# Optimization experiments

Hardware: AMD Instinct MI355X
Metric: run time of the kernel (lower is better)

Reference implementation:

```python
import jax, jax.numpy as jnp
import numpy as np

S, B, NS, NC = 128, 64, 128, 8
D, Z, H, HI, NF = 32, 64, 128, 128, 2
N = NS * B
LOG2PI = float(np.log(2.0 * np.pi))
_m_in = np.arange(1, Z + 1)
_m_hid = (np.arange(HI) % (Z - 1)) + 1
MASK1 = jnp.asarray((_m_hid[None, :] >= _m_in[:, None]).astype(np.float32))  # [Z,HI]
MASK2 = jnp.asarray((_m_in[None, :] > _m_hid[:, None]).astype(np.float32))   # [HI,Z]


def setup_inputs() -> dict:
    key = jax.random.key(0)
    ks = jax.random.split(key, 16)
    r = lambda i, shape: jax.random.normal(ks[i], shape, jnp.float32) * 0.1
    return dict(
        input=jax.random.normal(ks[0], (S, B, D), jnp.float32),
        eps=jax.random.normal(ks[1], (S, N, Z), jnp.float32),
        u=jax.random.uniform(ks[2], (S, 3, NC, NS, B), dtype=jnp.float32),
        Wxh=r(3, (D, H)), Wzh=r(4, (Z, H)), bh=jnp.zeros(H, jnp.float32),
        Wg=r(5, (H, Z)), bg=jnp.zeros(Z, jnp.float32),
        Wp=r(6, (H, Z)), bp=jnp.zeros(Z, jnp.float32),
        Wz=r(7, (Z, Z)), bz=jnp.zeros(Z, jnp.float32),
        Wsc=r(8, (Z, Z)), bsc=jnp.zeros(Z, jnp.float32),
        iaf_W1=r(9, (NF, Z, HI)), iaf_b1=jnp.zeros((NF, HI), jnp.float32),
        iaf_Wm=r(10, (NF, HI, Z)), iaf_bm=jnp.zeros((NF, Z), jnp.float32),
        iaf_Ws=r(11, (NF, HI, Z)), iaf_bs=jnp.zeros((NF, Z), jnp.float32),
        We1=r(12, (Z, H)), be1=jnp.zeros(H, jnp.float32),
        We2=r(13, (H, 4 * NC)), be2=jnp.zeros(4 * NC, jnp.float32),
    )


def _forward(input, eps, u, Wxh, Wzh, bh, Wg, bg, Wp, bp, Wz, bz, Wsc, bsc,
             iaf_W1, iaf_b1, iaf_Wm, iaf_bm, iaf_Ws, iaf_bs, We1, be1, We2, be2):
    def step(z_prev, inp):
        x, eps_t, u_t = inp                        # x:[B,D] eps_t:[N,Z] u_t:[3,NC,NS,B]
        xr = jnp.tile(x, (NS, 1))                  # == input[i].repeat(n_samples, 1) -> [N,D]
        # GatedTransition
        h = jax.nn.relu(xr @ Wxh + z_prev @ Wzh + bh)
        gate = jax.nn.sigmoid(h @ Wg + bg)
        prop = h @ Wp + bp
        loc = (1.0 - gate) * (z_prev @ Wz + bz) + gate * prop
        scale = jax.nn.softplus(jax.nn.relu(prop) @ Wsc + bsc) + 1e-3
        # base rsample + log_prob of base sample (eps form)
        z = loc + scale * eps_t
        base_lp = jnp.sum(-0.5 * eps_t * eps_t - jnp.log(scale) - 0.5 * LOG2PI, axis=-1)
        # IAF stack: y = sigma*x + (1-sigma)*mu, cached log_prob = base_lp - sum log sigma
        logdet = jnp.zeros((N,), z.dtype)
        for f in range(NF):
            hh = jax.nn.relu(z @ (iaf_W1[f] * MASK1) + iaf_b1[f])
            mu = hh @ (iaf_Wm[f] * MASK2) + iaf_bm[f]
            sg = jax.nn.sigmoid(hh @ (iaf_Ws[f] * MASK2) + iaf_bs[f] + 1.0)
            z = sg * z + (1.0 - sg) * mu
            logdet = logdet + jnp.sum(jnp.log(sg), axis=-1)
        z_lp = (base_lp - logdet).reshape(NS, B)
        # Emitter -> [N, 4*NC]; .t().view(4,NC,NS,B).split([3,1])
        e = jax.nn.relu(z @ We1 + be1) @ We2 + be2
        et = e.T.reshape(4, NC, NS, B)
        logits, frac = et[:3], jax.nn.sigmoid(et[3:4])
        samp = (u_t < jax.nn.sigmoid(logits)).astype(jnp.float32)  # Bernoulli sample
        x_lp = samp * jax.nn.log_sigmoid(logits) + (1.0 - samp) * jax.nn.log_sigmoid(-logits)
        return z, (samp, frac, x_lp, z_lp)

    z0 = jnp.zeros((N, Z), input.dtype)
    _, (samples, fractions, x_logprobs, z_logprobs) = jax.lax.scan(step, z0, (input, eps, u))
    return samples, fractions, x_logprobs, z_logprobs


def reference(input, eps, u, Wxh, Wzh, bh, Wg, bg, Wp, bp, Wz, bz, Wsc, bsc,
              iaf_W1, iaf_b1, iaf_Wm, iaf_bm, iaf_Ws, iaf_bs, We1, be1, We2, be2):
    return _forward(input, eps, u, Wxh, Wzh, bh, Wg, bg, Wp, bp, Wz, bz, Wsc, bsc,
                    iaf_W1, iaf_b1, iaf_Wm, iaf_bm, iaf_Ws, iaf_bs, We1, be1, We2, be2)
```

## Files before the change

kernel.cpp:

```cpp
#include <hip/hip_runtime.h>


typedef _Float16 f16x8 __attribute__((ext_vector_type(8)));
typedef _Float16 f16x4 __attribute__((ext_vector_type(4)));
typedef float    f32x4 __attribute__((ext_vector_type(4)));
typedef unsigned short u16;

#define MFMA16(a,b,c) __builtin_amdgcn_mfma_f32_16x16x32_f16((a),(b),(c),0,0,0)

namespace {
constexpr int S = 128;
constexpr long FRAC_OFF = 25165824L;
constexpr long XLP_OFF  = 33554432L;
constexpr long ZLP_OFF  = 58720256L;
constexpr float HLOG2PI = 0.91893853320467274f;
constexpr float INVLO   = 1.0f / 2048.0f;

constexpr int C1HI = 0,      C1LO = 12288;
constexpr int GPHI = 24576,  GPLO = 40960;
constexpr int WZHI = 57344,  WZLO = 61440;
constexpr int SCHI = 65536,  SCLO = 69632;
constexpr int W1B  = 73728;
constexpr int MSB  = 106496;
constexpr int E1HI = 172032, E1LO = 180224;
constexpr int E2HI = 188416, E2LO = 192512;
constexpr int XHI  = 196608, XLO  = 458752;
}

__device__ __forceinline__ float sigm(float x)      { return 1.0f / (1.0f + __expf(-x)); }
__device__ __forceinline__ float softplusf_(float x){ return fmaxf(x, 0.f) + __logf(1.f + __expf(-fabsf(x))); }
__device__ __forceinline__ float logsigm(float x)   { return fminf(x, 0.f) - __logf(1.f + __expf(-fabsf(x))); }

__device__ __forceinline__ void split2(float v, _Float16& hi, _Float16& lo) {
    hi = (_Float16)v;
    lo = (_Float16)((v - (float)hi) * 2048.0f);
}

__device__ __forceinline__ f16x8 rdA(const u16* t, int row, int k, int strideEls, int swm) {
    int byte = ((row * strideEls + k) * 2) ^ ((row & swm) << 4);
    return *(const f16x8*)((const char*)t + byte);
}
__device__ __forceinline__ f16x8 ldB(const u16* wa, int base, int col, int K, int koff) {
    return *(const f16x8*)(wa + base + col * K + koff);
}
__device__ __forceinline__ f16x8 ldLo(const u16* lds, int el, int col) {
    int byte = (el * 2) ^ ((col & 7) << 4);
    return *(const f16x8*)((const char*)lds + byte);
}

template<int NKS, int STRIDE, int SWM>
__device__ __forceinline__ void mmDual(const u16* Th, const u16* Tl, int lnc, int kf,
                                       const f16x8 (&wh)[NKS], const f16x8 (&wl)[NKS],
                                       float bias, f32x4& H0, f32x4& L0, f32x4& H1, f32x4& L1)
{
    H0 = (f32x4){bias, bias, bias, bias}; H1 = H0;
    L0 = (f32x4){0.f, 0.f, 0.f, 0.f};     L1 = L0;
#pragma unroll
    for (int ks = 0; ks < NKS; ++ks) {
        int k = ks * 32 + kf;
        f16x8 a0h = rdA(Th, lnc,      k, STRIDE, SWM);
        f16x8 a0l = rdA(Tl, lnc,      k, STRIDE, SWM);
        f16x8 a1h = rdA(Th, 16 + lnc, k, STRIDE, SWM);
        f16x8 a1l = rdA(Tl, 16 + lnc, k, STRIDE, SWM);
        H0 = MFMA16(a0h, wh[ks], H0); L0 = MFMA16(a0h, wl[ks], L0); L0 = MFMA16(a0l, wh[ks], L0);
        H1 = MFMA16(a1h, wh[ks], H1); L1 = MFMA16(a1h, wl[ks], L1); L1 = MFMA16(a1l, wh[ks], L1);
    }
}

template<bool RELU>
__device__ __forceinline__ void stAct(f32x4 H, f32x4 L, int rt, int lng, int col,
                                      u16* th, u16* tl, int strideEls, int swm)
{
#pragma unroll
    for (int q = 0; q < 4; ++q) {
        int row = rt * 16 + lng * 4 + q;
        float v = H[q] + L[q] * INVLO;
        if (RELU) v = fmaxf(v, 0.f);
        _Float16 hi, lo; split2(v, hi, lo);
        int byte = ((row * strideEls + col) * 2) ^ ((row & swm) << 4);
        *(_Float16*)((char*)th + byte) = hi;
        *(_Float16*)((char*)tl + byte) = lo;
    }
}
__device__ __forceinline__ void stScr(f32x4 H, f32x4 L, int rt, int lng, int col,
                                      float* s, int strideEls)
{
#pragma unroll
    for (int q = 0; q < 4; ++q) {
        int row = rt * 16 + lng * 4 + q;
        int byte = ((row * strideEls + col) * 4) ^ ((row & 7) << 4);
        *(float*)((char*)s + byte) = H[q] + L[q] * INVLO;
    }
}
__device__ __forceinline__ f32x4 rdS4(const float* s, int strideEls, int row, int c) {
    int byte = ((row * strideEls + c) * 4) ^ ((row & 7) << 4);
    return *(const f32x4*)((const char*)s + byte);
}
__device__ __forceinline__ float rdS1(const float* s, int strideEls, int row, int c) {
    int byte = ((row * strideEls + c) * 4) ^ ((row & 7) << 4);
    return *(const float*)((const char*)s + byte);
}
__device__ __forceinline__ void wrS4(float* s, int strideEls, int row, int c, f32x4 v) {
    int byte = ((row * strideEls + c) * 4) ^ ((row & 7) << 4);
    *(f32x4*)((char*)s + byte) = v;
}
__device__ __forceinline__ void wrF16x4(u16* t, int strideEls, int row, int c, f16x4 v) {
    int byte = ((row * strideEls + c) * 2) ^ ((row & 7) << 4);
    *(f16x4*)((char*)t + byte) = v;
}
__device__ __forceinline__ f16x4 rdF16x4(const u16* t, int strideEls, int row, int c) {
    int byte = ((row * strideEls + c) * 2) ^ ((row & 7) << 4);
    return *(const f16x4*)((const char*)t + byte);
}

__global__ void prep_kernel(const float* __restrict__ input,
                            const float* __restrict__ Wxh, const float* __restrict__ Wzh,
                            const float* __restrict__ Wg,  const float* __restrict__ Wp,
                            const float* __restrict__ Wz,  const float* __restrict__ Wsc,
                            const float* __restrict__ W1,  const float* __restrict__ Wm,
                            const float* __restrict__ Ws_, const float* __restrict__ We1,
                            const float* __restrict__ We2, u16* __restrict__ wa)
{
    int idx = blockIdx.x * 256 + threadIdx.x;
    if (idx < 98304) {
        int hio = 0, loo = 0; float v = 0.f;
        int i = idx;
        if (i < 12288) {
            int col = i / 96, k = i % 96;
            v = (k < 32) ? Wxh[k * 128 + col] : Wzh[(k - 32) * 128 + col];
            hio = C1HI + i; loo = C1LO + i;
        } else if (i < 28672) { int j = i - 12288;
            int col = j >> 7, k = j & 127;
            v = (col < 64) ? Wg[k * 64 + col] : Wp[k * 64 + col - 64];
            hio = GPHI + j; loo = GPLO + j;
        } else if (i < 32768) { int j = i - 28672;
            int col = j >> 6, k = j & 63; v = Wz[k * 64 + col];
            hio = WZHI + j; loo = WZLO + j;
        } else if (i < 36864) { int j = i - 32768;
            int col = j >> 6, k = j & 63; v = Wsc[k * 64 + col];
            hio = SCHI + j; loo = SCLO + j;
        } else if (i < 53248) { int j = i - 36864;
            int f = j >> 13, jj = j & 8191;
            int col = jj >> 6, k = jj & 63;
            v = W1[(f * 64 + k) * 128 + col] * (((col % 63) >= k) ? 1.f : 0.f);
            hio = W1B + f * 16384 + jj; loo = hio + 8192;
        } else if (i < 86016) { int j = i - 53248;
            int f = j >> 14, jj = j & 16383;
            int col = jj >> 7, k = jj & 127;
            if (col < 64) v = Wm[(f * 128 + k) * 64 + col] * (((k % 63) < col) ? 1.f : 0.f);
            else { int c = col - 64;
                   v = Ws_[(f * 128 + k) * 64 + c]         * (((k % 63) < c)   ? 1.f : 0.f); }
            hio = MSB + f * 32768 + jj; loo = hio + 16384;
        } else if (i < 94208) { int j = i - 86016;
            int col = j >> 6, k = j & 63; v = We1[k * 128 + col];
            hio = E1HI + j; loo = E1LO + j;
        } else { int j = i - 94208;
            int col = j >> 7, k = j & 127; v = We2[k * 32 + col];
            hio = E2HI + j; loo = E2LO + j;
        }
        _Float16 hi, lo; split2(v, hi, lo);
        wa[hio] = __builtin_bit_cast(u16, hi);
        wa[loo] = __builtin_bit_cast(u16, lo);
    } else {
        int j = idx - 98304;
        if (j < 262144) {
            float v = input[j];
            _Float16 hi, lo; split2(v, hi, lo);
            wa[XHI + j] = __builtin_bit_cast(u16, hi);
            wa[XLO + j] = __builtin_bit_cast(u16, lo);
        }
    }
}

__global__ __launch_bounds__(512, 2)
void ssm_mfma_kernel(const float* __restrict__ eps, const float* __restrict__ u,
                     const float* __restrict__ bh,  const float* __restrict__ bg,
                     const float* __restrict__ bp,  const float* __restrict__ bz,
                     const float* __restrict__ bsc, const float* __restrict__ b1,
                     const float* __restrict__ bm,  const float* __restrict__ bs,
                     const float* __restrict__ be1, const float* __restrict__ be2,
                     const u16* __restrict__ wa, float* __restrict__ out)
{
    __shared__ u16 tXh[32 * 32],  tXl[32 * 32];
    __shared__ u16 tZh[32 * 64],  tZl[32 * 64];
    __shared__ u16 tHh[32 * 128], tHl[32 * 128];
    __shared__ u16 tPh[32 * 64],  tPl[32 * 64];
    __shared__ float scrB[32 * 128];
    __shared__ float scrZ[32 * 64];
    __shared__ float lpS[32][16];
    __shared__ u16 loMS[32768];
    __shared__ u16 loGP[16384];

    const int tid = threadIdx.x;
    const int ln  = tid & 63, w = tid >> 6;
    const int lnc = ln & 15, lng = ln >> 4;
    const int r0  = blockIdx.x * 32, b0 = r0 & 63;
    const int kf  = lng * 8;
    const int col0  = w * 16 + lnc;
    const int colz  = (w & 3) * 16 + lnc;
    const int colE2 = (w & 1) * 16 + lnc;
    const int khE2  = w >> 1;
    const int crow  = tid >> 4, ccol4 = (tid & 15) * 4;
    const int erow  = tid & 31, c0 = (tid >> 5) * 2;

    for (int i8 = tid; i8 < 4096; i8 += 512) {
        int el = i8 * 8;
        int f = el >> 14, rem = el & 16383, col = rem >> 7;
        f16x8 v = *(const f16x8*)(wa + MSB + f * 32768 + 16384 + rem);
        int byte = (el * 2) ^ ((col & 7) << 4);
        *(f16x8*)((char*)loMS + byte) = v;
    }
    for (int i8 = tid; i8 < 2048; i8 += 512) {
        int el = i8 * 8;
        int col = el >> 7;
        f16x8 v = *(const f16x8*)(wa + GPLO + el);
        int byte = (el * 2) ^ ((col & 7) << 4);
        *(f16x8*)((char*)loGP + byte) = v;
    }

    f16x8 wC1h[3], wC1l[3], wGPh[4], wZSh[2], wZSl[2];
    f16x8 wW1h[2][2], wW1l[2][2], wMSh[2][4];
    f16x8 wE1h[2], wE1l[2], wE2h[1], wE2l[1];
#pragma unroll
    for (int ks = 0; ks < 3; ++ks) {
        wC1h[ks] = ldB(wa, C1HI, col0, 96, ks * 32 + kf);
        wC1l[ks] = ldB(wa, C1LO, col0, 96, ks * 32 + kf);
    }
#pragma unroll
    for (int ks = 0; ks < 4; ++ks) {
        wGPh[ks] = ldB(wa, GPHI, col0, 128, ks * 32 + kf);
    }
    if (w < 4) {
#pragma unroll
        for (int ks = 0; ks < 2; ++ks) {
            wZSh[ks] = ldB(wa, WZHI, colz, 64, ks * 32 + kf);
            wZSl[ks] = ldB(wa, WZLO, colz, 64, ks * 32 + kf);
        }
    } else {
#pragma unroll
        for (int ks = 0; ks < 2; ++ks) {
            wZSh[ks] = ldB(wa, SCHI, colz, 64, ks * 32 + kf);
            wZSl[ks] = ldB(wa, SCLO, colz, 64, ks * 32 + kf);
        }
    }
#pragma unroll
    for (int f = 0; f < 2; ++f) {
#pragma unroll
        for (int ks = 0; ks < 2; ++ks) {
            wW1h[f][ks] = ldB(wa, W1B + f * 16384,        col0, 64, ks * 32 + kf);
            wW1l[f][ks] = ldB(wa, W1B + f * 16384 + 8192, col0, 64, ks * 32 + kf);
        }
#pragma unroll
        for (int ks = 0; ks < 4; ++ks) {
            wMSh[f][ks] = ldB(wa, MSB + f * 32768, col0, 128, ks * 32 + kf);
        }
    }
#pragma unroll
    for (int ks = 0; ks < 2; ++ks) {
        wE1h[ks] = ldB(wa, E1HI, col0, 64, ks * 32 + kf);
        wE1l[ks] = ldB(wa, E1LO, col0, 64, ks * 32 + kf);
    }
    wE2h[0] = ldB(wa, E2HI, colE2, 128, khE2 * 32 + kf);
    wE2l[0] = ldB(wa, E2LO, colE2, 128, khE2 * 32 + kf);

    const float bhv  = bh[col0];
    const float bGPv = (col0 < 64) ? bg[col0] : bp[col0 - 64];
    const float bzsv = (w < 4) ? bz[colz] : bsc[colz];
    float bW1v[2], bMSv[2];
#pragma unroll
    for (int f = 0; f < 2; ++f) {
        bW1v[f] = b1[f * 128 + col0];
        bMSv[f] = (col0 < 64) ? bm[f * 64 + col0] : bs[f * 64 + col0 - 64];
    }
    const float bE1v = be1[col0];
    const float bE2v = (khE2 == 0) ? be2[colE2] : 0.f;

    for (int i = tid; i < 32 * 64; i += 512) { tZh[i] = 0; tZl[i] = 0; }
    {
        int rr = tid >> 4, d2 = (tid & 15) * 2;
        int ge = (b0 + rr) * 32 + d2;
        unsigned xh = *(const unsigned*)(wa + XHI + ge);
        unsigned xl = *(const unsigned*)(wa + XLO + ge);
        int byte = (rr * 64 + d2 * 2) ^ ((rr & 3) << 4);
        *(unsigned*)((char*)tXh + byte) = xh;
        *(unsigned*)((char*)tXl + byte) = xl;
    }
    __syncthreads();

    for (int t = 0; t < S; ++t) {
        f32x4 epsv;

        {
            f32x4 H0 = {bhv, bhv, bhv, bhv}, H1 = H0;
            f32x4 L0 = {0.f, 0.f, 0.f, 0.f}, L1 = L0;
            {
                f16x8 a0h = rdA(tXh, lnc, kf, 32, 3),      a0l = rdA(tXl, lnc, kf, 32, 3);
                f16x8 a1h = rdA(tXh, 16 + lnc, kf, 32, 3), a1l = rdA(tXl, 16 + lnc, kf, 32, 3);
                H0 = MFMA16(a0h, wC1h[0], H0); L0 = MFMA16(a0h, wC1l[0], L0); L0 = MFMA16(a0l, wC1h[0], L0);
                H1 = MFMA16(a1h, wC1h[0], H1); L1 = MFMA16(a1h, wC1l[0], L1); L1 = MFMA16(a1l, wC1h[0], L1);
            }
#pragma unroll
            for (int ks = 1; ks < 3; ++ks) {
                int k = (ks - 1) * 32 + kf;
                f16x8 a0h = rdA(tZh, lnc, k, 64, 7),      a0l = rdA(tZl, lnc, k, 64, 7);
                f16x8 a1h = rdA(tZh, 16 + lnc, k, 64, 7), a1l = rdA(tZl, 16 + lnc, k, 64, 7);
                H0 = MFMA16(a0h, wC1h[ks], H0); L0 = MFMA16(a0h, wC1l[ks], L0); L0 = MFMA16(a0l, wC1h[ks], L0);
                H1 = MFMA16(a1h, wC1h[ks], H1); L1 = MFMA16(a1h, wC1l[ks], L1); L1 = MFMA16(a1l, wC1h[ks], L1);
            }
            stAct<true>(H0, L0, 0, lng, col0, tHh, tHl, 128, 7);
            stAct<true>(H1, L1, 1, lng, col0, tHh, tHl, 128, 7);
        }
        if (w < 4) {
            f32x4 H0, L0, H1, L1;
            mmDual<2, 64, 7>(tZh, tZl, lnc, kf, wZSh, wZSl, bzsv, H0, L0, H1, L1);
            stScr(H0, L0, 0, lng, colz, scrZ, 64);
            stScr(H1, L1, 1, lng, colz, scrZ, 64);
        }
        __syncthreads();

        {
            f32x4 H0 = {bGPv, bGPv, bGPv, bGPv}, H1 = H0;
            f32x4 L0 = {0.f, 0.f, 0.f, 0.f}, L1 = L0;
#pragma unroll
            for (int ks = 0; ks < 4; ++ks) {
                int k = ks * 32 + kf;
                f16x8 a0h = rdA(tHh, lnc, k, 128, 7),      a0l = rdA(tHl, lnc, k, 128, 7);
                f16x8 a1h = rdA(tHh, 16 + lnc, k, 128, 7), a1l = rdA(tHl, 16 + lnc, k, 128, 7);
                f16x8 bhf = wGPh[ks];
                f16x8 blf = ldLo(loGP, col0 * 128 + k, col0);
                H0 = MFMA16(a0h, bhf, H0); L0 = MFMA16(a0h, blf, L0); L0 = MFMA16(a0l, bhf, L0);
                H1 = MFMA16(a1h, bhf, H1); L1 = MFMA16(a1h, blf, L1); L1 = MFMA16(a1l, bhf, L1);
            }
            stScr(H0, L0, 0, lng, col0, scrB, 128);
            stScr(H1, L1, 1, lng, col0, scrB, 128);
        }
        __syncthreads();

        {
            epsv = *(const f32x4*)(eps + ((size_t)t * 8192 + r0 + crow) * 64 + ccol4);
            f32x4 gp4 = rdS4(scrB, 128, crow, ccol4);
            f32x4 pr4 = rdS4(scrB, 128, crow, 64 + ccol4);
            f32x4 zw4 = rdS4(scrZ, 64, crow, ccol4);
            f32x4 loc4; f16x4 ph4, pl4;
#pragma unroll
            for (int i = 0; i < 4; ++i) {
                float g = sigm(gp4[i]);
                loc4[i] = (1.f - g) * zw4[i] + g * pr4[i];
                float rp = fmaxf(pr4[i], 0.f);
                _Float16 hi, lo; split2(rp, hi, lo); ph4[i] = hi; pl4[i] = lo;
            }
            wrS4(scrB, 128, crow, 64 + ccol4, loc4);
            wrF16x4(tPh, 64, crow, ccol4, ph4);
            wrF16x4(tPl, 64, crow, ccol4, pl4);
        }
        __syncthreads();

        if (w >= 4) {
            f32x4 H0, L0, H1, L1;
            mmDual<2, 64, 7>(tPh, tPl, lnc, kf, wZSh, wZSl, bzsv, H0, L0, H1, L1);
            stScr(H0, L0, 0, lng, colz, scrB, 128);
            stScr(H1, L1, 1, lng, colz, scrB, 128);
        }
        __syncthreads();

        float lp = 0.f;
        {
            f32x4 s4   = rdS4(scrB, 128, crow, ccol4);
            f32x4 loc4 = rdS4(scrB, 128, crow, 64 + ccol4);
            f16x4 zh4, zl4;
#pragma unroll
            for (int i = 0; i < 4; ++i) {
                float sc = softplusf_(s4[i]) + 0.001f;
                float zv = loc4[i] + sc * epsv[i];
                lp += -0.5f * epsv[i] * epsv[i] - __logf(sc) - HLOG2PI;
                _Float16 hi, lo; split2(zv, hi, lo); zh4[i] = hi; zl4[i] = lo;
            }
            wrF16x4(tZh, 64, crow, ccol4, zh4);
            wrF16x4(tZl, 64, crow, ccol4, zl4);
        }
        __syncthreads();

#pragma unroll
        for (int f = 0; f < 2; ++f) {
            {
                f32x4 H0, L0, H1, L1;
                mmDual<2, 64, 7>(tZh, tZl, lnc, kf, wW1h[f], wW1l[f], bW1v[f], H0, L0, H1, L1);
                stAct<true>(H0, L0, 0, lng, col0, tHh, tHl, 128, 7);
                stAct<true>(H1, L1, 1, lng, col0, tHh, tHl, 128, 7);
            }
            __syncthreads();
            {
                f32x4 H0 = {bMSv[f], bMSv[f], bMSv[f], bMSv[f]}, H1 = H0;
                f32x4 L0 = {0.f, 0.f, 0.f, 0.f}, L1 = L0;
#pragma unroll
                for (int ks = 0; ks < 4; ++ks) {
                    int k = ks * 32 + kf;
                    f16x8 a0h = rdA(tHh, lnc, k, 128, 7),      a0l = rdA(tHl, lnc, k, 128, 7);
                    f16x8 a1h = rdA(tHh, 16 + lnc, k, 128, 7), a1l = rdA(tHl, 16 + lnc, k, 128, 7);
                    f16x8 bhf = wMSh[f][ks];
                    f16x8 blf = ldLo(loMS, f * 16384 + col0 * 128 + k, col0);
                    H0 = MFMA16(a0h, bhf, H0); L0 = MFMA16(a0h, blf, L0); L0 = MFMA16(a0l, bhf, L0);
                    H1 = MFMA16(a1h, bhf, H1); L1 = MFMA16(a1h, blf, L1); L1 = MFMA16(a1l, bhf, L1);
                }
                stScr(H0, L0, 0, lng, col0, scrB, 128);
                stScr(H1, L1, 1, lng, col0, scrB, 128);
            }
            __syncthreads();
            {
                f32x4 mu4 = rdS4(scrB, 128, crow, ccol4);
                f32x4 sp4 = rdS4(scrB, 128, crow, 64 + ccol4);
                f16x4 zh4 = rdF16x4(tZh, 64, crow, ccol4);
                f16x4 zl4 = rdF16x4(tZl, 64, crow, ccol4);
                f16x4 nzh, nzl;
#pragma unroll
                for (int i = 0; i < 4; ++i) {
                    float zv = (float)zh4[i] + (float)zl4[i] * INVLO;
                    float sg = sigm(sp4[i] + 1.0f);
                    float zn = sg * zv + (1.f - sg) * mu4[i];
                    lp -= __logf(sg);
                    _Float16 hi, lo; split2(zn, hi, lo); nzh[i] = hi; nzl[i] = lo;
                }
                wrF16x4(tZh, 64, crow, ccol4, nzh);
                wrF16x4(tZl, 64, crow, ccol4, nzl);
                if (f == 1) lpS[crow][tid & 15] = lp;
            }
            __syncthreads();
        }

        {
            f32x4 H0, L0, H1, L1;
            mmDual<2, 64, 7>(tZh, tZl, lnc, kf, wE1h, wE1l, bE1v, H0, L0, H1, L1);
            stAct<true>(H0, L0, 0, lng, col0, tHh, tHl, 128, 7);
            stAct<true>(H1, L1, 1, lng, col0, tHh, tHl, 128, 7);
        }
        __syncthreads();

        {
            f32x4 H0, L0, H1, L1;
            H0 = (f32x4){bE2v, bE2v, bE2v, bE2v}; H1 = H0;
            L0 = (f32x4){0.f, 0.f, 0.f, 0.f};     L1 = L0;
            int k = khE2 * 32 + kf;
            f16x8 a0h = rdA(tHh, lnc, k, 128, 7),      a0l = rdA(tHl, lnc, k, 128, 7);
            f16x8 a1h = rdA(tHh, 16 + lnc, k, 128, 7), a1l = rdA(tHl, 16 + lnc, k, 128, 7);
            H0 = MFMA16(a0h, wE2h[0], H0); L0 = MFMA16(a0h, wE2l[0], L0); L0 = MFMA16(a0l, wE2h[0], L0);
            H1 = MFMA16(a1h, wE2h[0], H1); L1 = MFMA16(a1h, wE2l[0], L1); L1 = MFMA16(a1l, wE2h[0], L1);
            stScr(H0, L0, 0, lng, khE2 * 32 + colE2, scrB, 128);
            stScr(H1, L1, 1, lng, khE2 * 32 + colE2, scrB, 128);
        }
        if (t + 1 < S) {
            int rr = tid >> 4, d2 = (tid & 15) * 2;
            int ge = ((t + 1) * 64 + b0 + rr) * 32 + d2;
            unsigned xh = *(const unsigned*)(wa + XHI + ge);
            unsigned xl = *(const unsigned*)(wa + XLO + ge);
            int byte = (rr * 64 + d2 * 2) ^ ((rr & 3) << 4);
            *(unsigned*)((char*)tXh + byte) = xh;
            *(unsigned*)((char*)tXl + byte) = xl;
        }
        __syncthreads();

        {
#pragma unroll
            for (int q = 0; q < 2; ++q) {
                int col = c0 + q;
                float v = 0.f;
#pragma unroll
                for (int kh = 0; kh < 4; ++kh) v += rdS1(scrB, 128, erow, kh * 32 + col);
                if (col < 24) {
                    long plane = ((long)(t * 3 + (col >> 3)) * 8 + (col & 7)) * 8192 + r0 + erow;
                    float uvq = u[plane];
                    float sg = sigm(v);
                    bool hit = uvq < sg;
                    out[plane] = hit ? 1.f : 0.f;
                    out[XLP_OFF + plane] = hit ? logsigm(v) : logsigm(-v);
                } else {
                    long pf = ((long)t * 8 + (col & 7)) * 8192 + r0 + erow;
                    out[FRAC_OFF + pf] = sigm(v);
                }
            }
            if (tid < 32) {
                float s = 0.f;
#pragma unroll
                for (int g2 = 0; g2 < 16; ++g2) s += lpS[tid][g2];
                out[ZLP_OFF + (long)t * 8192 + r0 + tid] = s;
            }
        }
    }
}

extern "C" void kernel_launch(void* const* d_in, const int* in_sizes, int n_in,
                              void* d_out, int out_size, void* d_ws, size_t ws_size,
                              hipStream_t stream)
{
    const float* input = (const float*)d_in[0];
    const float* eps   = (const float*)d_in[1];
    const float* u     = (const float*)d_in[2];
    const float* Wxh   = (const float*)d_in[3];
    const float* Wzh   = (const float*)d_in[4];
    const float* bh    = (const float*)d_in[5];
    const float* Wg    = (const float*)d_in[6];
    const float* bg    = (const float*)d_in[7];
    const float* Wp    = (const float*)d_in[8];
    const float* bp    = (const float*)d_in[9];
    const float* Wz    = (const float*)d_in[10];
    const float* bz    = (const float*)d_in[11];
    const float* Wsc   = (const float*)d_in[12];
    const float* bsc   = (const float*)d_in[13];
    const float* W1    = (const float*)d_in[14];
    const float* b1    = (const float*)d_in[15];
    const float* Wm    = (const float*)d_in[16];
    const float* bm    = (const float*)d_in[17];
    const float* Ws    = (const float*)d_in[18];
    const float* bs    = (const float*)d_in[19];
    const float* We1   = (const float*)d_in[20];
    const float* be1   = (const float*)d_in[21];
    const float* We2   = (const float*)d_in[22];
    const float* be2   = (const float*)d_in[23];

    u16* wa = (u16*)d_ws;

    hipLaunchKernelGGL(prep_kernel, dim3(1408), dim3(256), 0, stream,
                       input, Wxh, Wzh, Wg, Wp, Wz, Wsc, W1, Wm, Ws, We1, We2, wa);

    hipLaunchKernelGGL(ssm_mfma_kernel, dim3(256), dim3(512), 0, stream,
                       eps, u, bh, bg, bp, bz, bsc, b1, bm, bs, be1, be2,
                       wa, (float*)d_out);
}
```

Before: 3.253 ms.

## Halve block size to 4 waves, each wave computing two column tiles

Shrinks the recurrent kernel from 8 to 4 waves per block, so each wave now owns two 16-column MFMA tiles and reuses each A-fragment LDS read across both. The Wz and Wsc projections are now done by all waves rather than split by wave halves, the emitter K-split changes from 4 to 2, and elementwise stages handle 8 columns per thread. This is meant to cut LDS A-operand traffic and barrier cost per timestep in a latency-bound serial loop. The trade-off is more register pressure from doubled weight fragments and less parallelism per CU.

```diff
diff --git a/kernel.cpp b/kernel.cpp
--- a/kernel.cpp
+++ b/kernel.cpp
@@ -5,6 +5,7 @@
 typedef _Float16 f16x4 __attribute__((ext_vector_type(4)));
 typedef float    f32x4 __attribute__((ext_vector_type(4)));
 typedef unsigned short u16;
+typedef unsigned long long u64;
 
 #define MFMA16(a,b,c) __builtin_amdgcn_mfma_f32_16x16x32_f16((a),(b),(c),0,0,0)
 
@@ -172,7 +173,7 @@
     }
 }
 
-__global__ __launch_bounds__(512, 2)
+__global__ __launch_bounds__(256, 1)
 void ssm_mfma_kernel(const float* __restrict__ eps, const float* __restrict__ u,
                      const float* __restrict__ bh,  const float* __restrict__ bg,
                      const float* __restrict__ bp,  const float* __restrict__ bz,
@@ -187,7 +188,7 @@
     __shared__ u16 tPh[32 * 64],  tPl[32 * 64];
     __shared__ float scrB[32 * 128];
     __shared__ float scrZ[32 * 64];
-    __shared__ float lpS[32][16];
+    __shared__ float lpS[32][9];
     __shared__ u16 loMS[32768];
     __shared__ u16 loGP[16384];
 
@@ -196,21 +197,22 @@
     const int lnc = ln & 15, lng = ln >> 4;
     const int r0  = blockIdx.x * 32, b0 = r0 & 63;
     const int kf  = lng * 8;
-    const int col0  = w * 16 + lnc;
-    const int colz  = (w & 3) * 16 + lnc;
+    const int ct0   = w * 32 + lnc;
+    const int ct1   = ct0 + 16;
+    const int colz  = w * 16 + lnc;
     const int colE2 = (w & 1) * 16 + lnc;
     const int khE2  = w >> 1;
-    const int crow  = tid >> 4, ccol4 = (tid & 15) * 4;
-    const int erow  = tid & 31, c0 = (tid >> 5) * 2;
-
-    for (int i8 = tid; i8 < 4096; i8 += 512) {
+    const int crow  = tid >> 3, cc = (tid & 7) * 8;
+    const int erow  = tid & 31, cg = (tid >> 5) * 4;
+
+    for (int i8 = tid; i8 < 4096; i8 += 256) {
         int el = i8 * 8;
         int f = el >> 14, rem = el & 16383, col = rem >> 7;
         f16x8 v = *(const f16x8*)(wa + MSB + f * 32768 + 16384 + rem);
         int byte = (el * 2) ^ ((col & 7) << 4);
         *(f16x8*)((char*)loMS + byte) = v;
     }
-    for (int i8 = tid; i8 < 2048; i8 += 512) {
+    for (int i8 = tid; i8 < 2048; i8 += 256) {
         int el = i8 * 8;
         int col = el >> 7;
         f16x8 v = *(const f16x8*)(wa + GPLO + el);
@@ -218,253 +220,348 @@
         *(f16x8*)((char*)loGP + byte) = v;
     }
 
-    f16x8 wC1h[3], wC1l[3], wGPh[4], wZSh[2], wZSl[2];
-    f16x8 wW1h[2][2], wW1l[2][2], wMSh[2][4];
-    f16x8 wE1h[2], wE1l[2], wE2h[1], wE2l[1];
-#pragma unroll
-    for (int ks = 0; ks < 3; ++ks) {
-        wC1h[ks] = ldB(wa, C1HI, col0, 96, ks * 32 + kf);
-        wC1l[ks] = ldB(wa, C1LO, col0, 96, ks * 32 + kf);
-    }
-#pragma unroll
-    for (int ks = 0; ks < 4; ++ks) {
-        wGPh[ks] = ldB(wa, GPHI, col0, 128, ks * 32 + kf);
-    }
-    if (w < 4) {
+    f16x8 wC1h[2][3], wC1l[2][3];
+    f16x8 wGPh[2][4];
+    f16x8 wWZh[2], wWZl[2], wSCh[2], wSCl[2];
+    f16x8 wW1h[2][2][2], wW1l[2][2][2];
+    f16x8 wMSh[2][2][4];
+    f16x8 wE1h[2][2], wE1l[2][2];
+    f16x8 wE2h[2], wE2l[2];
+#pragma unroll
+    for (int j = 0; j < 2; ++j) {
+        int colj = ct0 + j * 16;
+#pragma unroll
+        for (int ks = 0; ks < 3; ++ks) {
+            wC1h[j][ks] = ldB(wa, C1HI, colj, 96, ks * 32 + kf);
+            wC1l[j][ks] = ldB(wa, C1LO, colj, 96, ks * 32 + kf);
+        }
+#pragma unroll
+        for (int ks = 0; ks < 4; ++ks)
+            wGPh[j][ks] = ldB(wa, GPHI, colj, 128, ks * 32 + kf);
 #pragma unroll
         for (int ks = 0; ks < 2; ++ks) {
-            wZSh[ks] = ldB(wa, WZHI, colz, 64, ks * 32 + kf);
-            wZSl[ks] = ldB(wa, WZLO, colz, 64, ks * 32 + kf);
-        }
-    } else {
-#pragma unroll
-        for (int ks = 0; ks < 2; ++ks) {
-            wZSh[ks] = ldB(wa, SCHI, colz, 64, ks * 32 + kf);
-            wZSl[ks] = ldB(wa, SCLO, colz, 64, ks * 32 + kf);
-        }
-    }
-#pragma unroll
-    for (int f = 0; f < 2; ++f) {
-#pragma unroll
-        for (int ks = 0; ks < 2; ++ks) {
-            wW1h[f][ks] = ldB(wa, W1B + f * 16384,        col0, 64, ks * 32 + kf);
-            wW1l[f][ks] = ldB(wa, W1B + f * 16384 + 8192, col0, 64, ks * 32 + kf);
-        }
-#pragma unroll
-        for (int ks = 0; ks < 4; ++ks) {
-            wMSh[f][ks] = ldB(wa, MSB + f * 32768, col0, 128, ks * 32 + kf);
+            wE1h[j][ks] = ldB(wa, E1HI, colj, 64, ks * 32 + kf);
+            wE1l[j][ks] = ldB(wa, E1LO, colj, 64, ks * 32 + kf);
+        }
+#pragma unroll
+        for (int f = 0; f < 2; ++f) {
+#pragma unroll
+            for (int ks = 0; ks < 2; ++ks) {
+                wW1h[f][j][ks] = ldB(wa, W1B + f * 16384,        colj, 64, ks * 32 + kf);
+                wW1l[f][j][ks] = ldB(wa, W1B + f * 16384 + 8192, colj, 64, ks * 32 + kf);
+            }
+#pragma unroll
+            for (int ks = 0; ks < 4; ++ks)
+                wMSh[f][j][ks] = ldB(wa, MSB + f * 32768, colj, 128, ks * 32 + kf);
         }
     }
 #pragma unroll
     for (int ks = 0; ks < 2; ++ks) {
-        wE1h[ks] = ldB(wa, E1HI, col0, 64, ks * 32 + kf);
-        wE1l[ks] = ldB(wa, E1LO, col0, 64, ks * 32 + kf);
-    }
-    wE2h[0] = ldB(wa, E2HI, colE2, 128, khE2 * 32 + kf);
-    wE2l[0] = ldB(wa, E2LO, colE2, 128, khE2 * 32 + kf);
-
-    const float bhv  = bh[col0];
-    const float bGPv = (col0 < 64) ? bg[col0] : bp[col0 - 64];
-    const float bzsv = (w < 4) ? bz[colz] : bsc[colz];
-    float bW1v[2], bMSv[2];
-#pragma unroll
-    for (int f = 0; f < 2; ++f) {
-        bW1v[f] = b1[f * 128 + col0];
-        bMSv[f] = (col0 < 64) ? bm[f * 64 + col0] : bs[f * 64 + col0 - 64];
-    }
-    const float bE1v = be1[col0];
+        wWZh[ks] = ldB(wa, WZHI, colz, 64, ks * 32 + kf);
+        wWZl[ks] = ldB(wa, WZLO, colz, 64, ks * 32 + kf);
+        wSCh[ks] = ldB(wa, SCHI, colz, 64, ks * 32 + kf);
+        wSCl[ks] = ldB(wa, SCLO, colz, 64, ks * 32 + kf);
+        wE2h[ks] = ldB(wa, E2HI, colE2, 128, khE2 * 64 + ks * 32 + kf);
+        wE2l[ks] = ldB(wa, E2LO, colE2, 128, khE2 * 64 + ks * 32 + kf);
+    }
+
+    float bhv[2], bGPv[2], bW1v[2][2], bMSv[2][2], bE1v[2];
+#pragma unroll
+    for (int j = 0; j < 2; ++j) {
+        int colj = ct0 + j * 16;
+        bhv[j]  = bh[colj];
+        bGPv[j] = (colj < 64) ? bg[colj] : bp[colj - 64];
+        bE1v[j] = be1[colj];
+#pragma unroll
+        for (int f = 0; f < 2; ++f) {
+            bW1v[f][j] = b1[f * 128 + colj];
+            bMSv[f][j] = (colj < 64) ? bm[f * 64 + colj] : bs[f * 64 + colj - 64];
+        }
+    }
+    const float bzv  = bz[colz];
+    const float bscv = bsc[colz];
     const float bE2v = (khE2 == 0) ? be2[colE2] : 0.f;
 
-    for (int i = tid; i < 32 * 64; i += 512) { tZh[i] = 0; tZl[i] = 0; }
+    for (int i = tid; i < 32 * 64; i += 256) { tZh[i] = 0; tZl[i] = 0; }
     {
-        int rr = tid >> 4, d2 = (tid & 15) * 2;
-        int ge = (b0 + rr) * 32 + d2;
-        unsigned xh = *(const unsigned*)(wa + XHI + ge);
-        unsigned xl = *(const unsigned*)(wa + XLO + ge);
-        int byte = (rr * 64 + d2 * 2) ^ ((rr & 3) << 4);
-        *(unsigned*)((char*)tXh + byte) = xh;
-        *(unsigned*)((char*)tXl + byte) = xl;
+        int rr = tid >> 3, d4 = (tid & 7) * 4;
+        int ge = (b0 + rr) * 32 + d4;
+        u64 xh = *(const u64*)(wa + XHI + ge);
+        u64 xl = *(const u64*)(wa + XLO + ge);
+        int byte = (rr * 64 + d4 * 2) ^ ((rr & 3) << 4);
+        *(u64*)((char*)tXh + byte) = xh;
+        *(u64*)((char*)tXl + byte) = xl;
     }
     __syncthreads();
 
     for (int t = 0; t < S; ++t) {
-        f32x4 epsv;
-
-        {
-            f32x4 H0 = {bhv, bhv, bhv, bhv}, H1 = H0;
-            f32x4 L0 = {0.f, 0.f, 0.f, 0.f}, L1 = L0;
-            {
-                f16x8 a0h = rdA(tXh, lnc, kf, 32, 3),      a0l = rdA(tXl, lnc, kf, 32, 3);
-                f16x8 a1h = rdA(tXh, 16 + lnc, kf, 32, 3), a1l = rdA(tXl, 16 + lnc, kf, 32, 3);
-                H0 = MFMA16(a0h, wC1h[0], H0); L0 = MFMA16(a0h, wC1l[0], L0); L0 = MFMA16(a0l, wC1h[0], L0);
-                H1 = MFMA16(a1h, wC1h[0], H1); L1 = MFMA16(a1h, wC1l[0], L1); L1 = MFMA16(a1l, wC1h[0], L1);
-            }
-#pragma unroll
-            for (int ks = 1; ks < 3; ++ks) {
-                int k = (ks - 1) * 32 + kf;
-                f16x8 a0h = rdA(tZh, lnc, k, 64, 7),      a0l = rdA(tZl, lnc, k, 64, 7);
-                f16x8 a1h = rdA(tZh, 16 + lnc, k, 64, 7), a1l = rdA(tZl, 16 + lnc, k, 64, 7);
-                H0 = MFMA16(a0h, wC1h[ks], H0); L0 = MFMA16(a0h, wC1l[ks], L0); L0 = MFMA16(a0l, wC1h[ks], L0);
-                H1 = MFMA16(a1h, wC1h[ks], H1); L1 = MFMA16(a1h, wC1l[ks], L1); L1 = MFMA16(a1l, wC1h[ks], L1);
-            }
-            stAct<true>(H0, L0, 0, lng, col0, tHh, tHl, 128, 7);
-            stAct<true>(H1, L1, 1, lng, col0, tHh, tHl, 128, 7);
-        }
-        if (w < 4) {
-            f32x4 H0, L0, H1, L1;
-            mmDual<2, 64, 7>(tZh, tZl, lnc, kf, wZSh, wZSl, bzsv, H0, L0, H1, L1);
-            stScr(H0, L0, 0, lng, colz, scrZ, 64);
-            stScr(H1, L1, 1, lng, colz, scrZ, 64);
+        f32x4 epsA, epsB;
+
+        {
+            f32x4 H[2], L[2], H1[2], L1[2];
+#pragma unroll
+            for (int j = 0; j < 2; ++j) {
+                H[j]  = (f32x4){bhv[j], bhv[j], bhv[j], bhv[j]};
+                H1[j] = H[j];
+                L[j]  = (f32x4){0.f, 0.f, 0.f, 0.f};
+                L1[j] = L[j];
+            }
+#pragma unroll
+            for (int ks = 0; ks < 3; ++ks) {
+                f16x8 a0h, a0l, a1h, a1l;
+                if (ks == 0) {
+                    a0h = rdA(tXh, lnc, kf, 32, 3);      a0l = rdA(tXl, lnc, kf, 32, 3);
+                    a1h = rdA(tXh, 16 + lnc, kf, 32, 3); a1l = rdA(tXl, 16 + lnc, kf, 32, 3);
+                } else {
+                    int k = (ks - 1) * 32 + kf;
+                    a0h = rdA(tZh, lnc, k, 64, 7);       a0l = rdA(tZl, lnc, k, 64, 7);
+                    a1h = rdA(tZh, 16 + lnc, k, 64, 7);  a1l = rdA(tZl, 16 + lnc, k, 64, 7);
+                }
+#pragma unroll
+                for (int j = 0; j < 2; ++j) {
+                    H[j]  = MFMA16(a0h, wC1h[j][ks], H[j]);  L[j]  = MFMA16(a0h, wC1l[j][ks], L[j]);  L[j]  = MFMA16(a0l, wC1h[j][ks], L[j]);
+                    H1[j] = MFMA16(a1h, wC1h[j][ks], H1[j]); L1[j] = MFMA16(a1h, wC1l[j][ks], L1[j]); L1[j] = MFMA16(a1l, wC1h[j][ks], L1[j]);
+                }
+            }
+#pragma unroll
+            for (int j = 0; j < 2; ++j) {
+                stAct<true>(H[j],  L[j],  0, lng, ct0 + j * 16, tHh, tHl, 128, 7);
+                stAct<true>(H1[j], L1[j], 1, lng, ct0 + j * 16, tHh, tHl, 128, 7);
+            }
+        }
+        {
+            f32x4 ZH0, ZL0, ZH1, ZL1;
+            mmDual<2, 64, 7>(tZh, tZl, lnc, kf, wWZh, wWZl, bzv, ZH0, ZL0, ZH1, ZL1);
+            stScr(ZH0, ZL0, 0, lng, colz, scrZ, 64);
+            stScr(ZH1, ZL1, 1, lng, colz, scrZ, 64);
         }
         __syncthreads();
 
         {
-            f32x4 H0 = {bGPv, bGPv, bGPv, bGPv}, H1 = H0;
-            f32x4 L0 = {0.f, 0.f, 0.f, 0.f}, L1 = L0;
+            f32x4 H[2], L[2], H1[2], L1[2];
+#pragma unroll
+            for (int j = 0; j < 2; ++j) {
+                H[j]  = (f32x4){bGPv[j], bGPv[j], bGPv[j], bGPv[j]};
+                H1[j] = H[j];
+                L[j]  = (f32x4){0.f, 0.f, 0.f, 0.f};
+                L1[j] = L[j];
+            }
 #pragma unroll
             for (int ks = 0; ks < 4; ++ks) {
                 int k = ks * 32 + kf;
                 f16x8 a0h = rdA(tHh, lnc, k, 128, 7),      a0l = rdA(tHl, lnc, k, 128, 7);
                 f16x8 a1h = rdA(tHh, 16 + lnc, k, 128, 7), a1l = rdA(tHl, 16 + lnc, k, 128, 7);
-                f16x8 bhf = wGPh[ks];
-                f16x8 blf = ldLo(loGP, col0 * 128 + k, col0);
-                H0 = MFMA16(a0h, bhf, H0); L0 = MFMA16(a0h, blf, L0); L0 = MFMA16(a0l, bhf, L0);
-                H1 = MFMA16(a1h, bhf, H1); L1 = MFMA16(a1h, blf, L1); L1 = MFMA16(a1l, bhf, L1);
-            }
-            stScr(H0, L0, 0, lng, col0, scrB, 128);
-            stScr(H1, L1, 1, lng, col0, scrB, 128);
+#pragma unroll
+                for (int j = 0; j < 2; ++j) {
+                    int colj = ct0 + j * 16;
+                    f16x8 bhf = wGPh[j][ks];
+                    f16x8 blf = ldLo(loGP, colj * 128 + k, colj);
+                    H[j]  = MFMA16(a0h, bhf, H[j]);  L[j]  = MFMA16(a0h, blf, L[j]);  L[j]  = MFMA16(a0l, bhf, L[j]);
+                    H1[j] = MFMA16(a1h, bhf, H1[j]); L1[j] = MFMA16(a1h, blf, L1[j]); L1[j] = MFMA16(a1l, bhf, L1[j]);
+                }
+            }
+#pragma unroll
+            for (int j = 0; j < 2; ++j) {
+                stScr(H[j],  L[j],  0, lng, ct0 + j * 16, scrB, 128);
+                stScr(H1[j], L1[j], 1, lng, ct0 + j * 16, scrB, 128);
+            }
         }
         __syncthreads();
 
         {
-            epsv = *(const f32x4*)(eps + ((size_t)t * 8192 + r0 + crow) * 64 + ccol4);
-            f32x4 gp4 = rdS4(scrB, 128, crow, ccol4);
-            f32x4 pr4 = rdS4(scrB, 128, crow, 64 + ccol4);
-            f32x4 zw4 = rdS4(scrZ, 64, crow, ccol4);
-            f32x4 loc4; f16x4 ph4, pl4;
-#pragma unroll
-            for (int i = 0; i < 4; ++i) {
-                float g = sigm(gp4[i]);
-                loc4[i] = (1.f - g) * zw4[i] + g * pr4[i];
-                float rp = fmaxf(pr4[i], 0.f);
-                _Float16 hi, lo; split2(rp, hi, lo); ph4[i] = hi; pl4[i] = lo;
-            }
-            wrS4(scrB, 128, crow, 64 + ccol4, loc4);
-            wrF16x4(tPh, 64, crow, ccol4, ph4);
-            wrF16x4(tPl, 64, crow, ccol4, pl4);
+            epsA = *(const f32x4*)(eps + ((size_t)t * 8192 + r0 + crow) * 64 + cc);
+            epsB = *(const f32x4*)(eps + ((size_t)t * 8192 + r0 + crow) * 64 + cc + 4);
+#pragma unroll
+            for (int h4 = 0; h4 < 2; ++h4) {
+                int c4 = cc + h4 * 4;
+                f32x4 gp4 = rdS4(scrB, 128, crow, c4);
+                f32x4 pr4 = rdS4(scrB, 128, crow, 64 + c4);
+                f32x4 zw4 = rdS4(scrZ, 64, crow, c4);
+                f32x4 loc4; f16x4 ph4, pl4;
+#pragma unroll
+                for (int i = 0; i < 4; ++i) {
+                    float g = sigm(gp4[i]);
+                    loc4[i] = (1.f - g) * zw4[i] + g * pr4[i];
+                    float rp = fmaxf(pr4[i], 0.f);
+                    _Float16 hi, lo; split2(rp, hi, lo); ph4[i] = hi; pl4[i] = lo;
+                }
+                wrS4(scrB, 128, crow, 64 + c4, loc4);
+                wrF16x4(tPh, 64, crow, c4, ph4);
+                wrF16x4(tPl, 64, crow, c4, pl4);
+            }
         }
         __syncthreads();
 
-        if (w >= 4) {
-            f32x4 H0, L0, H1, L1;
-            mmDual<2, 64, 7>(tPh, tPl, lnc, kf, wZSh, wZSl, bzsv, H0, L0, H1, L1);
-            stScr(H0, L0, 0, lng, colz, scrB, 128);
-            stScr(H1, L1, 1, lng, colz, scrB, 128);
+        {
+            f32x4 SH0, SL0, SH1, SL1;
+            mmDual<2, 64, 7>(tPh, tPl, lnc, kf, wSCh, wSCl, bscv, SH0, SL0, SH1, SL1);
+            stScr(SH0, SL0, 0, lng, colz, scrB, 128);
+            stScr(SH1, SL1, 1, lng, colz, scrB, 128);
         }
         __syncthreads();
 
         float lp = 0.f;
-        {
-            f32x4 s4   = rdS4(scrB, 128, crow, ccol4);
-            f32x4 loc4 = rdS4(scrB, 128, crow, 64 + ccol4);
+#pragma unroll
+        for (int h4 = 0; h4 < 2; ++h4) {
+            int c4 = cc + h4 * 4;
+            f32x4 ev   = (h4 == 0) ? epsA : epsB;
+            f32x4 s4   = rdS4(scrB, 128, crow, c4);
+            f32x4 loc4 = rdS4(scrB, 128, crow, 64 + c4);
             f16x4 zh4, zl4;
 #pragma unroll
             for (int i = 0; i < 4; ++i) {
                 float sc = softplusf_(s4[i]) + 0.001f;
-                float zv = loc4[i] + sc * epsv[i];
-                lp += -0.5f * epsv[i] * epsv[i] - __logf(sc) - HLOG2PI;
+                float zv = loc4[i] + sc * ev[i];
+                lp += -0.5f * ev[i] * ev[i] - __logf(sc) - HLOG2PI;
                 _Float16 hi, lo; split2(zv, hi, lo); zh4[i] = hi; zl4[i] = lo;
             }
-            wrF16x4(tZh, 64, crow, ccol4, zh4);
-            wrF16x4(tZl, 64, crow, ccol4, zl4);
+            wrF16x4(tZh, 64, crow, c4, zh4);
+            wrF16x4(tZl, 64, crow, c4, zl4);
         }
         __syncthreads();
 
 #pragma unroll
         for (int f = 0; f < 2; ++f) {
             {
-                f32x4 H0, L0, H1, L1;
-                mmDual<2, 64, 7>(tZh, tZl, lnc, kf, wW1h[f], wW1l[f], bW1v[f], H0, L0, H1, L1);
-                stAct<true>(H0, L0, 0, lng, col0, tHh, tHl, 128, 7);
-                stAct<true>(H1, L1, 1, lng, col0, tHh, tHl, 128, 7);
+                f32x4 H[2], L[2], H1[2], L1[2];
+#pragma unroll
+                for (int j = 0; j < 2; ++j) {
+                    H[j]  = (f32x4){bW1v[f][j], bW1v[f][j], bW1v[f][j], bW1v[f][j]};
+                    H1[j] = H[j];
+                    L[j]  = (f32x4){0.f, 0.f, 0.f, 0.f};
+                    L1[j] = L[j];
+                }
+#pragma unroll
+                for (int ks = 0; ks < 2; ++ks) {
+                    int k = ks * 32 + kf;
+                    f16x8 a0h = rdA(tZh, lnc, k, 64, 7),      a0l = rdA(tZl, lnc, k, 64, 7);
+                    f16x8 a1h = rdA(tZh, 16 + lnc, k, 64, 7), a1l = rdA(tZl, 16 + lnc, k, 64, 7);
+#pragma unroll
+                    for (int j = 0; j < 2; ++j) {
+                        H[j]  = MFMA16(a0h, wW1h[f][j][ks], H[j]);  L[j]  = MFMA16(a0h, wW1l[f][j][ks], L[j]);  L[j]  = MFMA16(a0l, wW1h[f][j][ks], L[j]);
+                        H1[j] = MFMA16(a1h, wW1h[f][j][ks], H1[j]); L1[j] = MFMA16(a1h, wW1l[f][j][ks], L1[j]); L1[j] = MFMA16(a1l, wW1h[f][j][ks], L1[j]);
+                    }
+                }
+#pragma unroll
+                for (int j = 0; j < 2; ++j) {
+                    stAct<true>(H[j],  L[j],  0, lng, ct0 + j * 16, tHh, tHl, 128, 7);
+                    stAct<true>(H1[j], L1[j], 1, lng, ct0 + j * 16, tHh, tHl, 128, 7);
+                }
             }
             __syncthreads();
             {
-                f32x4 H0 = {bMSv[f], bMSv[f], bMSv[f], bMSv[f]}, H1 = H0;
-                f32x4 L0 = {0.f, 0.f, 0.f, 0.f}, L1 = L0;
+                f32x4 H[2], L[2], H1[2], L1[2];
+#pragma unroll
+                for (int j = 0; j < 2; ++j) {
+                    H[j]  = (f32x4){bMSv[f][j], bMSv[f][j], bMSv[f][j], bMSv[f][j]};
+                    H1[j] = H[j];
+                    L[j]  = (f32x4){0.f, 0.f, 0.f, 0.f};
+                    L1[j] = L[j];
+                }
 #pragma unroll
                 for (int ks = 0; ks < 4; ++ks) {
                     int k = ks * 32 + kf;
                     f16x8 a0h = rdA(tHh, lnc, k, 128, 7),      a0l = rdA(tHl, lnc, k, 128, 7);
                     f16x8 a1h = rdA(tHh, 16 + lnc, k, 128, 7), a1l = rdA(tHl, 16 + lnc, k, 128, 7);
-                    f16x8 bhf = wMSh[f][ks];
-                    f16x8 blf = ldLo(loMS, f * 16384 + col0 * 128 + k, col0);
-                    H0 = MFMA16(a0h, bhf, H0); L0 = MFMA16(a0h, blf, L0); L0 = MFMA16(a0l, bhf, L0);
-                    H1 = MFMA16(a1h, bhf, H1); L1 = MFMA16(a1h, blf, L1); L1 = MFMA16(a1l, bhf, L1);
-                }
-                stScr(H0, L0, 0, lng, col0, scrB, 128);
-                stScr(H1, L1, 1, lng, col0, scrB, 128);
+#pragma unroll
+                    for (int j = 0; j < 2; ++j) {
+                        int colj = ct0 + j * 16;
+                        f16x8 bhf = wMSh[f][j][ks];
+                        f16x8 blf = ldLo(loMS, f * 16384 + colj * 128 + k, colj);
+                        H[j]  = MFMA16(a0h, bhf, H[j]);  L[j]  = MFMA16(a0h, blf, L[j]);  L[j]  = MFMA16(a0l, bhf, L[j]);
+                        H1[j] = MFMA16(a1h, bhf, H1[j]); L1[j] = MFMA16(a1h, blf, L1[j]); L1[j] = MFMA16(a1l, bhf, L1[j]);
+                    }
+                }
+#pragma unroll
+                for (int j = 0; j < 2; ++j) {
+                    stScr(H[j],  L[j],  0, lng, ct0 + j * 16, scrB, 128);
+                    stScr(H1[j], L1[j], 1, lng, ct0 + j * 16, scrB, 128);
+                }
             }
             __syncthreads();
             {
-                f32x4 mu4 = rdS4(scrB, 128, crow, ccol4);
-                f32x4 sp4 = rdS4(scrB, 128, crow, 64 + ccol4);
-                f16x4 zh4 = rdF16x4(tZh, 64, crow, ccol4);
-                f16x4 zl4 = rdF16x4(tZl, 64, crow, ccol4);
-                f16x4 nzh, nzl;
-#pragma unroll
-                for (int i = 0; i < 4; ++i) {
-                    float zv = (float)zh4[i] + (float)zl4[i] * INVLO;
-                    float sg = sigm(sp4[i] + 1.0f);
-                    float zn = sg * zv + (1.f - sg) * mu4[i];
-                    lp -= __logf(sg);
-                    _Float16 hi, lo; split2(zn, hi, lo); nzh[i] = hi; nzl[i] = lo;
-                }
-                wrF16x4(tZh, 64, crow, ccol4, nzh);
-                wrF16x4(tZl, 64, crow, ccol4, nzl);
-                if (f == 1) lpS[crow][tid & 15] = lp;
+#pragma unroll
+                for (int h4 = 0; h4 < 2; ++h4) {
+                    int c4 = cc + h4 * 4;
+                    f32x4 mu4 = rdS4(scrB, 128, crow, c4);
+                    f32x4 sp4 = rdS4(scrB, 128, crow, 64 + c4);
+                    f16x4 zh4 = rdF16x4(tZh, 64, crow, c4);
+                    f16x4 zl4 = rdF16x4(tZl, 64, crow, c4);
+                    f16x4 nzh, nzl;
+#pragma unroll
+                    for (int i = 0; i < 4; ++i) {
+                        float zv = (float)zh4[i] + (float)zl4[i] * INVLO;
+                        float sg = sigm(sp4[i] + 1.0f);
+                        float zn = sg * zv + (1.f - sg) * mu4[i];
+                        lp -= __logf(sg);
+                        _Float16 hi, lo; split2(zn, hi, lo); nzh[i] = hi; nzl[i] = lo;
+                    }
+                    wrF16x4(tZh, 64, crow, c4, nzh);
+                    wrF16x4(tZl, 64, crow, c4, nzl);
+                }
+                if (f == 1) lpS[crow][tid & 7] = lp;
             }
             __syncthreads();
         }
 
         {
-            f32x4 H0, L0, H1, L1;
-            mmDual<2, 64, 7>(tZh, tZl, lnc, kf, wE1h, wE1l, bE1v, H0, L0, H1, L1);
-            stAct<true>(H0, L0, 0, lng, col0, tHh, tHl, 128, 7);
-            stAct<true>(H1, L1, 1, lng, col0, tHh, tHl, 128, 7);
+            f32x4 H[2], L[2], H1[2], L1[2];
+#pragma unroll
+            for (int j = 0; j < 2; ++j) {
+                H[j]  = (f32x4){bE1v[j], bE1v[j], bE1v[j], bE1v[j]};
+                H1[j] = H[j];
+                L[j]  = (f32x4){0.f, 0.f, 0.f, 0.f};
+                L1[j] = L[j];
+            }
+#pragma unroll
+            for (int ks = 0; ks < 2; ++ks) {
+                int k = ks * 32 + kf;
+                f16x8 a0h = rdA(tZh, lnc, k, 64, 7),      a0l = rdA(tZl, lnc, k, 64, 7);
+                f16x8 a1h = rdA(tZh, 16 + lnc, k, 64, 7), a1l = rdA(tZl, 16 + lnc, k, 64, 7);
+#pragma unroll
+                for (int j = 0; j < 2; ++j) {
+                    H[j]  = MFMA16(a0h, wE1h[j][ks], H[j]);  L[j]  = MFMA16(a0h, wE1l[j][ks], L[j]);  L[j]  = MFMA16(a0l, wE1h[j][ks], L[j]);
+                    H1[j] = MFMA16(a1h, wE1h[j][ks], H1[j]); L1[j] = MFMA16(a1h, wE1l[j][ks], L1[j]); L1[j] = MFMA16(a1l, wE1h[j][ks], L1[j]);
+                }
+            }
+#pragma unroll
+            for (int j = 0; j < 2; ++j) {
+                stAct<true>(H[j],  L[j],  0, lng, ct0 + j * 16, tHh, tHl, 128, 7);
+                stAct<true>(H1[j], L1[j], 1, lng, ct0 + j * 16, tHh, tHl, 128, 7);
+            }
         }
         __syncthreads();
 
         {
-            f32x4 H0, L0, H1, L1;
-            H0 = (f32x4){bE2v, bE2v, bE2v, bE2v}; H1 = H0;
-            L0 = (f32x4){0.f, 0.f, 0.f, 0.f};     L1 = L0;
-            int k = khE2 * 32 + kf;
-            f16x8 a0h = rdA(tHh, lnc, k, 128, 7),      a0l = rdA(tHl, lnc, k, 128, 7);
-            f16x8 a1h = rdA(tHh, 16 + lnc, k, 128, 7), a1l = rdA(tHl, 16 + lnc, k, 128, 7);
-            H0 = MFMA16(a0h, wE2h[0], H0); L0 = MFMA16(a0h, wE2l[0], L0); L0 = MFMA16(a0l, wE2h[0], L0);
-            H1 = MFMA16(a1h, wE2h[0], H1); L1 = MFMA16(a1h, wE2l[0], L1); L1 = MFMA16(a1l, wE2h[0], L1);
-            stScr(H0, L0, 0, lng, khE2 * 32 + colE2, scrB, 128);
-            stScr(H1, L1, 1, lng, khE2 * 32 + colE2, scrB, 128);
+            f32x4 H0 = {bE2v, bE2v, bE2v, bE2v}, H1 = H0;
+            f32x4 L0 = {0.f, 0.f, 0.f, 0.f},     L1 = L0;
+#pragma unroll
+            for (int ks = 0; ks < 2; ++ks) {
+                int k = khE2 * 64 + ks * 32 + kf;
+                f16x8 a0h = rdA(tHh, lnc, k, 128, 7),      a0l = rdA(tHl, lnc, k, 128, 7);
+                f16x8 a1h = rdA(tHh, 16 + lnc, k, 128, 7), a1l = rdA(tHl, 16 + lnc, k, 128, 7);
+                H0 = MFMA16(a0h, wE2h[ks], H0); L0 = MFMA16(a0h, wE2l[ks], L0); L0 = MFMA16(a0l, wE2h[ks], L0);
+                H1 = MFMA16(a1h, wE2h[ks], H1); L1 = MFMA16(a1h, wE2l[ks], L1); L1 = MFMA16(a1l, wE2h[ks], L1);
+            }
+            stScr(H0, L0, 0, lng, khE2 * 64 + colE2, scrB, 128);
+            stScr(H1, L1, 1, lng, khE2 * 64 + colE2, scrB, 128);
         }
         if (t + 1 < S) {
-            int rr = tid >> 4, d2 = (tid & 15) * 2;
-            int ge = ((t + 1) * 64 + b0 + rr) * 32 + d2;
-            unsigned xh = *(const unsigned*)(wa + XHI + ge);
-            unsigned xl = *(const unsigned*)(wa + XLO + ge);
-            int byte = (rr * 64 + d2 * 2) ^ ((rr & 3) << 4);
-            *(unsigned*)((char*)tXh + byte) = xh;
-            *(unsigned*)((char*)tXl + byte) = xl;
+            int rr = tid >> 3, d4 = (tid & 7) * 4;
+            int ge = ((t + 1) * 64 + b0 + rr) * 32 + d4;
+            u64 xh = *(const u64*)(wa + XHI + ge);
+            u64 xl = *(const u64*)(wa + XLO + ge);
+            int byte = (rr * 64 + d4 * 2) ^ ((rr & 3) << 4);
+            *(u64*)((char*)tXh + byte) = xh;
+            *(u64*)((char*)tXl + byte) = xl;
         }
         __syncthreads();
 
         {
 #pragma unroll
-            for (int q = 0; q < 2; ++q) {
-                int col = c0 + q;
-                float v = 0.f;
-#pragma unroll
-                for (int kh = 0; kh < 4; ++kh) v += rdS1(scrB, 128, erow, kh * 32 + col);
+            for (int q = 0; q < 4; ++q) {
+                int col = cg + q;
+                float v = rdS1(scrB, 128, erow, col) + rdS1(scrB, 128, erow, 64 + col);
                 if (col < 24) {
                     long plane = ((long)(t * 3 + (col >> 3)) * 8 + (col & 7)) * 8192 + r0 + erow;
                     float uvq = u[plane];
@@ -480,7 +577,7 @@
             if (tid < 32) {
                 float s = 0.f;
 #pragma unroll
-                for (int g2 = 0; g2 < 16; ++g2) s += lpS[tid][g2];
+                for (int g2 = 0; g2 < 8; ++g2) s += lpS[tid][g2];
                 out[ZLP_OFF + (long)t * 8192 + r0 + tid] = s;
             }
         }
@@ -521,7 +618,7 @@
     hipLaunchKernelGGL(prep_kernel, dim3(1408), dim3(256), 0, stream,
                        input, Wxh, Wzh, Wg, Wp, Wz, Wsc, W1, Wm, Ws, We1, We2, wa);
 
-    hipLaunchKernelGGL(ssm_mfma_kernel, dim3(256), dim3(512), 0, stream,
+    hipLaunchKernelGGL(ssm_mfma_kernel, dim3(256), dim3(256), 0, stream,
                        eps, u, bh, bg, bp, bz, bsc, b1, bm, bs, be1, be2,
                        wa, (float*)d_out);
 }
```

Result: faster. 2.855 ms (-12.2%).
